# Kernel optimization log

Measured on AMD Instinct MI355X. Metric: run time of the kernel, lower is better.

The kernel has to match this reference:

```python
import jax, jax.numpy as jnp
import numpy as np

B, L, DK, DV, H = 2, 2048, 512, 512, 8
DH_K = DK // H  # 64
DH_V = DV // H  # 64


def setup_inputs() -> dict:
    key = jax.random.key(0)
    ks = jax.random.split(key, 6)
    scale_w = 1.0 / np.sqrt(DK)
    return {
        "keys": jax.random.normal(ks[0], (B, L, DK), dtype=jnp.float32),
        "queries": jax.random.normal(ks[1], (B, L, DK), dtype=jnp.float32),
        "values": jax.random.normal(ks[2], (B, L, DV), dtype=jnp.float32),
        "WQ": jax.random.normal(ks[3], (H, DK, DH_K), dtype=jnp.float32) * scale_w,
        "WK": jax.random.normal(ks[4], (H, DK, DH_K), dtype=jnp.float32) * scale_w,
        "WV": jax.random.normal(ks[5], (H, DV, DH_V), dtype=jnp.float32) * scale_w,
    }


def reference(keys, queries, values, WQ, WK, WV):
    # Per-head projections, vectorized over all H heads at once.
    Q = jnp.einsum('bld,hde->bhle', queries, WQ)   # [B,H,Lq,dh]
    K = jnp.einsum('bld,hde->bhle', keys, WK)      # [B,H,Lk,dh]
    V = jnp.einsum('bld,hde->bhle', values, WV)    # [B,H,Lk,dv_h]
    Lk = keys.shape[1]
    # NOTE: original scales by sqrt(seq_len_k), not sqrt(head_dim).
    y = jnp.einsum('bhqe,bhke->bhqk', Q, K) / jnp.sqrt(jnp.float32(Lk))
    # NOTE: original applies softmax over torch dim=1 of [B,Lq,Lk],
    # i.e. the QUERY axis (axis=2 here in [B,H,Lq,Lk]).
    z = jax.nn.softmax(y, axis=2)
    out = jnp.einsum('bhqk,bhke->bhqe', z, V)      # [B,H,Lq,dv_h]
    # Concat heads on the feature dim (same order as torch.concat(..., 2)).
    Bq, Hh, Lq, Dh = out.shape
    return out.transpose(0, 2, 1, 3).reshape(Bq, Lq, Hh * Dh)
```

## Files before the change

kernel.cpp:

```cpp
#include <hip/hip_runtime.h>
#include <hip/hip_bf16.h>

#define LL 2048
#define DM 512
#define SCALE 0.02209708691207961f

typedef unsigned short u16;
typedef __attribute__((ext_vector_type(8))) short short8;
typedef __attribute__((ext_vector_type(4))) short short4v;
typedef __attribute__((ext_vector_type(4))) float f32x4;

#define XAQ_OFF 0u
#define XAK_OFF 2097152u
#define WB_OFF  4194304u
#define QA_OFF  4980736u
#define KA_OFF  7077888u
#define VT_OFF  9175040u
#define VB_OFF  11272192u

__device__ __forceinline__ u16 f2bf(float f) {
  union { float f; unsigned u; } v; v.f = f;
  unsigned r = v.u + 0x7fff + ((v.u >> 16) & 1);
  return (u16)(r >> 16);
}
__device__ __forceinline__ float bf2f(u16 u) {
  union { unsigned u; float f; } v; v.u = ((unsigned)u) << 16; return v.f;
}
__device__ __forceinline__ size_t frag_idx(int bh, int t64, int w, int c, int lane) {
  return ((((size_t)(bh * 32 + t64) * 4 + w) * 2 + c) * 64 + lane) * 8;
}
__device__ __forceinline__ size_t vb_idx(int bh, int kt, int w, int et, int lane) {
  return ((((size_t)(bh * 32 + kt) * 4 + w) * 4 + et) * 64 + lane) * 4;
}

__global__ __launch_bounds__(256) void prep_kernel(
    const float* __restrict__ queries, const float* __restrict__ keys,
    const float* __restrict__ WQ, const float* __restrict__ WK,
    const float* __restrict__ WV, u16* __restrict__ wsb) {
  int t = threadIdx.x;
  if (blockIdx.x < 2048) {
    size_t c = (size_t)blockIdx.x * 256 + t;
    int tens = (int)(c >> 18);
    size_t off = (c & 262143u) * 8;
    int b  = (int)(off >> 20);
    int l  = (int)((off >> 9) & 2047);
    int d8 = (int)((off & 511) >> 3);
    int kt = d8 >> 2, quad = d8 & 3;
    const float* src = (tens ? keys : queries) + off;
    float4 a = *(const float4*)(src);
    float4 bb = *(const float4*)(src + 4);
    short8 o;
    o[0] = (short)f2bf(a.x); o[1] = (short)f2bf(a.y);
    o[2] = (short)f2bf(a.z); o[3] = (short)f2bf(a.w);
    o[4] = (short)f2bf(bb.x); o[5] = (short)f2bf(bb.y);
    o[6] = (short)f2bf(bb.z); o[7] = (short)f2bf(bb.w);
    size_t dst = (tens ? XAK_OFF : XAQ_OFF) +
        ((((size_t)b * 128 + (l >> 4)) * 16 + kt) * 64 + (quad * 16 + (l & 15))) * 8;
    *(short8*)(wsb + dst) = o;
  } else {
    int c2 = (blockIdx.x - 2048) * 256 + t;
    int lane = c2 & 63;
    int nt = (c2 >> 6) & 3;
    int kt = (c2 >> 8) & 15;
    int h  = (c2 >> 12) & 7;
    int z  = c2 >> 15;
    int quad = lane >> 4, l16 = lane & 15;
    const float* W = (z == 0) ? WQ : (z == 1) ? WK : WV;
    const float* src = W + ((size_t)h * DM + kt * 32 + quad * 8) * 64 + nt * 16 + l16;
    short8 o;
#pragma unroll
    for (int j = 0; j < 8; ++j) o[j] = (short)f2bf(src[(size_t)j * 64]);
    *(short8*)(wsb + WB_OFF + (size_t)c2 * 8) = o;
  }
}

__global__ __launch_bounds__(256) void proj_kernel(const float* __restrict__ values,
                                                   u16* __restrict__ wsb) {
  int t = threadIdx.x;
  int lane = t & 63, w = t >> 6, quad = lane >> 4, l16 = lane & 15;
  int z = blockIdx.z, bh = blockIdx.y, b = bh >> 3, h = bh & 7;
  int QT = blockIdx.x, qbase = QT * 64;

  const u16* Bw = wsb + WB_OFF + ((size_t)(z * 8 + h) * 16) * 4 * 64 * 8;
  __shared__ __align__(16) short As[64 * 40];

  f32x4 acc[4];
#pragma unroll
  for (int nt = 0; nt < 4; ++nt) acc[nt] = (f32x4){0.f, 0.f, 0.f, 0.f};

  if (z < 2) {
    const u16* Ab = wsb + ((z == 0) ? XAQ_OFF : XAK_OFF) +
        (((size_t)b * 128 + (qbase >> 4) + w) * 16) * 64 * 8;
#pragma unroll 4
    for (int kt = 0; kt < 16; ++kt) {
      short8 a = *(const short8*)(Ab + ((size_t)kt * 64 + lane) * 8);
#pragma unroll
      for (int nt = 0; nt < 4; ++nt) {
        short8 bb = *(const short8*)(Bw + (((size_t)kt * 4 + nt) * 64 + lane) * 8);
        acc[nt] = __builtin_amdgcn_mfma_f32_16x16x32_bf16(a, bb, acc[nt], 0, 0, 0);
      }
    }
  } else {
    const float* inbase = values + ((size_t)b * LL + qbase) * DM;
    for (int kt = 0; kt < 16; ++kt) {
      __syncthreads();
#pragma unroll
      for (int rep = 0; rep < 2; ++rep) {
        int f4 = t + rep * 256;
        int row = f4 >> 3, c4 = f4 & 7;
        float4 v = *(const float4*)(inbase + (size_t)row * DM + kt * 32 + c4 * 4);
        short* dst = &As[row * 40 + c4 * 4];
        dst[0] = (short)f2bf(v.x); dst[1] = (short)f2bf(v.y);
        dst[2] = (short)f2bf(v.z); dst[3] = (short)f2bf(v.w);
      }
      __syncthreads();
      short8 a = *(const short8*)&As[(w * 16 + l16) * 40 + quad * 8];
#pragma unroll
      for (int nt = 0; nt < 4; ++nt) {
        short8 bb = *(const short8*)(Bw + (((size_t)kt * 4 + nt) * 64 + lane) * 8);
        acc[nt] = __builtin_amdgcn_mfma_f32_16x16x32_bf16(a, bb, acc[nt], 0, 0, 0);
      }
    }
  }

  if (z < 2) {
    u16* base = wsb + ((z == 0) ? QA_OFF : KA_OFF);
    float sc = (z == 0) ? SCALE : 1.0f;
#pragma unroll
    for (int nt = 0; nt < 4; ++nt) {
      int c = nt >> 1;
      int quadp = (nt & 1) * 2 + (l16 >> 3);
      int j = l16 & 7;
#pragma unroll
      for (int r = 0; r < 4; ++r) {
        int lanep = quadp * 16 + quad * 4 + r;
        base[frag_idx(bh, QT, w, c, lanep) + j] = f2bf(acc[nt][r] * sc);
      }
    }
  } else {
    u16* og = wsb + VT_OFF + (size_t)bh * 64 * LL;
#pragma unroll
    for (int nt = 0; nt < 4; ++nt)
#pragma unroll
      for (int r = 0; r < 4; ++r)
        og[(size_t)(nt * 16 + l16) * LL + qbase + w * 16 + quad * 4 + r] = f2bf(acc[nt][r]);
  }
}

__global__ __launch_bounds__(256) void stats_kernel(u16* __restrict__ wsb) {
  int t = threadIdx.x;
  int lane = t & 63, w = t >> 6, quad = lane >> 4, l16 = lane & 15;
  int bh = blockIdx.y;
  int KT = blockIdx.x;

  short8 ka[4][2];
#pragma unroll
  for (int mt = 0; mt < 4; ++mt)
#pragma unroll
    for (int c = 0; c < 2; ++c)
      ka[mt][c] = *(const short8*)(wsb + KA_OFF + frag_idx(bh, KT, mt, c, lane));

  float rs[4][4];
#pragma unroll
  for (int mt = 0; mt < 4; ++mt)
#pragma unroll
    for (int r = 0; r < 4; ++r) rs[mt][r] = 0.f;

  for (int qt = 0; qt < 32; ++qt) {
    short8 qb0 = *(const short8*)(wsb + QA_OFF + frag_idx(bh, qt, w, 0, lane));
    short8 qb1 = *(const short8*)(wsb + QA_OFF + frag_idx(bh, qt, w, 1, lane));
#pragma unroll
    for (int mt = 0; mt < 4; ++mt) {
      f32x4 y = (f32x4){0.f, 0.f, 0.f, 0.f};
      y = __builtin_amdgcn_mfma_f32_16x16x32_bf16(ka[mt][0], qb0, y, 0, 0, 0);
      y = __builtin_amdgcn_mfma_f32_16x16x32_bf16(ka[mt][1], qb1, y, 0, 0, 0);
#pragma unroll
      for (int r = 0; r < 4; ++r) rs[mt][r] += __expf(y[r]);
    }
  }
#pragma unroll
  for (int mt = 0; mt < 4; ++mt)
#pragma unroll
    for (int r = 0; r < 4; ++r) {
      rs[mt][r] += __shfl_xor(rs[mt][r], 1);
      rs[mt][r] += __shfl_xor(rs[mt][r], 2);
      rs[mt][r] += __shfl_xor(rs[mt][r], 4);
      rs[mt][r] += __shfl_xor(rs[mt][r], 8);
    }

  __shared__ float Sred[4][64];
  __shared__ float Ss[64];
  if (l16 == 0) {
#pragma unroll
    for (int mt = 0; mt < 4; ++mt)
#pragma unroll
      for (int r = 0; r < 4; ++r)
        Sred[w][mt * 16 + quad * 4 + r] = rs[mt][r];
  }
  __syncthreads();
  if (t < 64) Ss[t] = 1.0f / (Sred[0][t] + Sred[1][t] + Sred[2][t] + Sred[3][t]);
  __syncthreads();

#pragma unroll
  for (int rep = 0; rep < 2; ++rep) {
    int f8 = t + rep * 256;
    int e = f8 >> 3, c8 = f8 & 7;
    const u16* src = wsb + VT_OFF + ((size_t)bh * 64 + e) * LL + KT * 64 + c8 * 8;
    short8 v = *(const short8*)src;
    float sv[8];
#pragma unroll
    for (int i = 0; i < 8; ++i) sv[i] = bf2f((u16)v[i]) * Ss[c8 * 8 + i];
    int wv = c8 >> 1, et = e >> 4;
#pragma unroll
    for (int g = 0; g < 2; ++g) {
      short4v o;
#pragma unroll
      for (int j = 0; j < 4; ++j) o[j] = (short)f2bf(sv[g * 4 + j]);
      int lanep = ((c8 & 1) * 2 + g) * 16 + (e & 15);
      *(short4v*)(wsb + VB_OFF + vb_idx(bh, KT, wv, et, lanep)) = o;
    }
  }
}

__global__ __launch_bounds__(256, 2) void attn_kernel(const u16* __restrict__ wsb,
                                                      float* __restrict__ out) {
  int t = threadIdx.x;
  int lane = t & 63, w = t >> 6, quad = lane >> 4, l16 = lane & 15;
  int bh = blockIdx.y, b = bh >> 3, h = bh & 7;
  int QT = blockIdx.x, qbase = QT * 64;

  short8 qf[4][2];
#pragma unroll
  for (int nt = 0; nt < 4; ++nt)
#pragma unroll
    for (int c = 0; c < 2; ++c)
      qf[nt][c] = *(const short8*)(wsb + QA_OFF + frag_idx(bh, QT, nt, c, lane));

  f32x4 oacc[4][4];
#pragma unroll
  for (int nt = 0; nt < 4; ++nt)
#pragma unroll
    for (int et = 0; et < 4; ++et) oacc[nt][et] = (f32x4){0.f, 0.f, 0.f, 0.f};

  for (int kt = 0; kt < 32; ++kt) {
    short8 ka0 = *(const short8*)(wsb + KA_OFF + frag_idx(bh, kt, w, 0, lane));
    short8 ka1 = *(const short8*)(wsb + KA_OFF + frag_idx(bh, kt, w, 1, lane));
    short4v vb[4];
#pragma unroll
    for (int et = 0; et < 4; ++et)
      vb[et] = *(const short4v*)(wsb + VB_OFF + vb_idx(bh, kt, w, et, lane));

#pragma unroll
    for (int nt = 0; nt < 4; ++nt) {
      f32x4 y = (f32x4){0.f, 0.f, 0.f, 0.f};
      y = __builtin_amdgcn_mfma_f32_16x16x32_bf16(ka0, qf[nt][0], y, 0, 0, 0);
      y = __builtin_amdgcn_mfma_f32_16x16x32_bf16(ka1, qf[nt][1], y, 0, 0, 0);
      short4v pa;
#pragma unroll
      for (int r = 0; r < 4; ++r) pa[r] = (short)f2bf(__expf(y[r]));
#pragma unroll
      for (int et = 0; et < 4; ++et)
        oacc[nt][et] = __builtin_amdgcn_mfma_f32_16x16x16bf16_1k(pa, vb[et], oacc[nt][et], 0, 0, 0);
    }
  }

  __shared__ float red[4][64][68];
#pragma unroll
  for (int nt = 0; nt < 4; ++nt)
#pragma unroll
    for (int et = 0; et < 4; ++et)
#pragma unroll
      for (int r = 0; r < 4; ++r)
        red[w][nt * 16 + quad * 4 + r][et * 16 + l16] = oacc[nt][et][r];
  __syncthreads();
  float* og = out + ((size_t)b * LL + qbase + w * 16) * 512 + h * 64;
#pragma unroll
  for (int i = 0; i < 16; ++i) {
    float s = red[0][w * 16 + i][lane] + red[1][w * 16 + i][lane] +
              red[2][w * 16 + i][lane] + red[3][w * 16 + i][lane];
    og[(size_t)i * 512 + lane] = s;
  }
}

extern "C" void kernel_launch(void* const* d_in, const int* in_sizes, int n_in,
                              void* d_out, int out_size, void* d_ws, size_t ws_size,
                              hipStream_t stream) {
  const float* keys    = (const float*)d_in[0];
  const float* queries = (const float*)d_in[1];
  const float* values  = (const float*)d_in[2];
  const float* WQ      = (const float*)d_in[3];
  const float* WK      = (const float*)d_in[4];
  const float* WV      = (const float*)d_in[5];
  float* out = (float*)d_out;
  u16* wsb = (u16*)d_ws;

  prep_kernel<<<dim3(2048 + 384), 256, 0, stream>>>(queries, keys, WQ, WK, WV, wsb);
  proj_kernel<<<dim3(32, 16, 3), 256, 0, stream>>>(values, wsb);
  stats_kernel<<<dim3(32, 16), 256, 0, stream>>>(wsb);
  attn_kernel<<<dim3(32, 16), 256, 0, stream>>>(wsb, out);
}
```

Baseline: 147.5 us.

## Pre-convert values to bf16 fragments and stage projection outputs through LDS

The prep kernel now converts all three inputs (queries, keys, values) into bf16 MFMA A-fragment layout using an LDS transpose with coalesced loads and stores. This lets the V projection use the same register-only MFMA loop instead of per-k-tile LDS staging with barriers. Projection outputs are staged in shared memory so Q/K fragments are written as short8 vectors and V goes straight into the VB fragment layout. The stats kernel then only rescales VB in place, and the VT intermediate is dropped. This trades scattered 2-byte stores and an extra transpose pass for one more LDS round trip and barrier in the projection epilogue.

```diff
diff --git a/kernel.cpp b/kernel.cpp
--- a/kernel.cpp
+++ b/kernel.cpp
@@ -12,10 +12,10 @@
 
 #define XAQ_OFF 0u
 #define XAK_OFF 2097152u
-#define WB_OFF  4194304u
-#define QA_OFF  4980736u
-#define KA_OFF  7077888u
-#define VT_OFF  9175040u
+#define XAV_OFF 4194304u
+#define WB_OFF  6291456u
+#define QA_OFF  7077888u
+#define KA_OFF  9175040u
 #define VB_OFF  11272192u
 
 __device__ __forceinline__ u16 f2bf(float f) {
@@ -35,30 +35,40 @@
 
 __global__ __launch_bounds__(256) void prep_kernel(
     const float* __restrict__ queries, const float* __restrict__ keys,
-    const float* __restrict__ WQ, const float* __restrict__ WK,
-    const float* __restrict__ WV, u16* __restrict__ wsb) {
-  int t = threadIdx.x;
-  if (blockIdx.x < 2048) {
-    size_t c = (size_t)blockIdx.x * 256 + t;
-    int tens = (int)(c >> 18);
-    size_t off = (c & 262143u) * 8;
-    int b  = (int)(off >> 20);
-    int l  = (int)((off >> 9) & 2047);
-    int d8 = (int)((off & 511) >> 3);
-    int kt = d8 >> 2, quad = d8 & 3;
-    const float* src = (tens ? keys : queries) + off;
-    float4 a = *(const float4*)(src);
-    float4 bb = *(const float4*)(src + 4);
-    short8 o;
-    o[0] = (short)f2bf(a.x); o[1] = (short)f2bf(a.y);
-    o[2] = (short)f2bf(a.z); o[3] = (short)f2bf(a.w);
-    o[4] = (short)f2bf(bb.x); o[5] = (short)f2bf(bb.y);
-    o[6] = (short)f2bf(bb.z); o[7] = (short)f2bf(bb.w);
-    size_t dst = (tens ? XAK_OFF : XAQ_OFF) +
-        ((((size_t)b * 128 + (l >> 4)) * 16 + kt) * 64 + (quad * 16 + (l & 15))) * 8;
-    *(short8*)(wsb + dst) = o;
+    const float* __restrict__ values, const float* __restrict__ WQ,
+    const float* __restrict__ WK, const float* __restrict__ WV,
+    u16* __restrict__ wsb) {
+  int t = threadIdx.x;
+  int blk = blockIdx.x;
+  if (blk < 768) {
+    int tens = blk >> 8;
+    int grp  = blk & 255;
+    const float* src = (tens == 0 ? queries : tens == 1 ? keys : values) +
+                       (size_t)grp * 16 * 512;
+    __shared__ __align__(16) u16 Xs[16][520];
+#pragma unroll
+    for (int rep = 0; rep < 8; ++rep) {
+      int f4 = t + rep * 256;
+      int row = f4 >> 7, c4 = f4 & 127;
+      float4 v = *(const float4*)(src + (size_t)row * 512 + c4 * 4);
+      short4v o;
+      o[0] = (short)f2bf(v.x); o[1] = (short)f2bf(v.y);
+      o[2] = (short)f2bf(v.z); o[3] = (short)f2bf(v.w);
+      *(short4v*)&Xs[row][c4 * 4] = o;
+    }
+    __syncthreads();
+    u16* dst = wsb + (tens == 0 ? XAQ_OFF : tens == 1 ? XAK_OFF : XAV_OFF) +
+               (size_t)grp * 16 * 64 * 8;
+#pragma unroll
+    for (int rep = 0; rep < 4; ++rep) {
+      int o = t + rep * 256;
+      int kt = o >> 6, lane = o & 63;
+      int quad = lane >> 4, l16 = lane & 15;
+      short8 v = *(const short8*)&Xs[l16][kt * 32 + quad * 8];
+      *(short8*)(dst + (size_t)o * 8) = v;
+    }
   } else {
-    int c2 = (blockIdx.x - 2048) * 256 + t;
+    int c2 = (blk - 768) * 256 + t;
     int lane = c2 & 63;
     int nt = (c2 >> 6) & 3;
     int kt = (c2 >> 8) & 15;
@@ -74,76 +84,58 @@
   }
 }
 
-__global__ __launch_bounds__(256) void proj_kernel(const float* __restrict__ values,
-                                                   u16* __restrict__ wsb) {
+__global__ __launch_bounds__(256) void proj_kernel(u16* __restrict__ wsb) {
   int t = threadIdx.x;
   int lane = t & 63, w = t >> 6, quad = lane >> 4, l16 = lane & 15;
   int z = blockIdx.z, bh = blockIdx.y, b = bh >> 3, h = bh & 7;
-  int QT = blockIdx.x, qbase = QT * 64;
+  int QT = blockIdx.x;
 
   const u16* Bw = wsb + WB_OFF + ((size_t)(z * 8 + h) * 16) * 4 * 64 * 8;
-  __shared__ __align__(16) short As[64 * 40];
+  const u16* Ab = wsb + (z == 0 ? XAQ_OFF : z == 1 ? XAK_OFF : XAV_OFF) +
+      (((size_t)b * 128 + QT * 4 + w) * 16) * 64 * 8;
 
   f32x4 acc[4];
 #pragma unroll
   for (int nt = 0; nt < 4; ++nt) acc[nt] = (f32x4){0.f, 0.f, 0.f, 0.f};
 
+#pragma unroll 4
+  for (int kt = 0; kt < 16; ++kt) {
+    short8 a = *(const short8*)(Ab + ((size_t)kt * 64 + lane) * 8);
+#pragma unroll
+    for (int nt = 0; nt < 4; ++nt) {
+      short8 bb = *(const short8*)(Bw + (((size_t)kt * 4 + nt) * 64 + lane) * 8);
+      acc[nt] = __builtin_amdgcn_mfma_f32_16x16x32_bf16(a, bb, acc[nt], 0, 0, 0);
+    }
+  }
+
+  __shared__ float Cs[64][68];
+  float sc = (z == 0) ? SCALE : 1.0f;
+#pragma unroll
+  for (int nt = 0; nt < 4; ++nt)
+#pragma unroll
+    for (int r = 0; r < 4; ++r)
+      Cs[w * 16 + quad * 4 + r][nt * 16 + l16] = acc[nt][r] * sc;
+  __syncthreads();
+
   if (z < 2) {
-    const u16* Ab = wsb + ((z == 0) ? XAQ_OFF : XAK_OFF) +
-        (((size_t)b * 128 + (qbase >> 4) + w) * 16) * 64 * 8;
-#pragma unroll 4
-    for (int kt = 0; kt < 16; ++kt) {
-      short8 a = *(const short8*)(Ab + ((size_t)kt * 64 + lane) * 8);
-#pragma unroll
-      for (int nt = 0; nt < 4; ++nt) {
-        short8 bb = *(const short8*)(Bw + (((size_t)kt * 4 + nt) * 64 + lane) * 8);
-        acc[nt] = __builtin_amdgcn_mfma_f32_16x16x32_bf16(a, bb, acc[nt], 0, 0, 0);
-      }
+    u16* base = wsb + (z == 0 ? QA_OFF : KA_OFF);
+#pragma unroll
+    for (int c = 0; c < 2; ++c) {
+      const float* srcr = &Cs[w * 16 + l16][c * 32 + quad * 8];
+      short8 o;
+#pragma unroll
+      for (int j = 0; j < 8; ++j) o[j] = (short)f2bf(srcr[j]);
+      *(short8*)(base + frag_idx(bh, QT, w, c, lane)) = o;
     }
   } else {
-    const float* inbase = values + ((size_t)b * LL + qbase) * DM;
-    for (int kt = 0; kt < 16; ++kt) {
-      __syncthreads();
-#pragma unroll
-      for (int rep = 0; rep < 2; ++rep) {
-        int f4 = t + rep * 256;
-        int row = f4 >> 3, c4 = f4 & 7;
-        float4 v = *(const float4*)(inbase + (size_t)row * DM + kt * 32 + c4 * 4);
-        short* dst = &As[row * 40 + c4 * 4];
-        dst[0] = (short)f2bf(v.x); dst[1] = (short)f2bf(v.y);
-        dst[2] = (short)f2bf(v.z); dst[3] = (short)f2bf(v.w);
-      }
-      __syncthreads();
-      short8 a = *(const short8*)&As[(w * 16 + l16) * 40 + quad * 8];
-#pragma unroll
-      for (int nt = 0; nt < 4; ++nt) {
-        short8 bb = *(const short8*)(Bw + (((size_t)kt * 4 + nt) * 64 + lane) * 8);
-        acc[nt] = __builtin_amdgcn_mfma_f32_16x16x32_bf16(a, bb, acc[nt], 0, 0, 0);
-      }
-    }
-  }
-
-  if (z < 2) {
-    u16* base = wsb + ((z == 0) ? QA_OFF : KA_OFF);
-    float sc = (z == 0) ? SCALE : 1.0f;
-#pragma unroll
-    for (int nt = 0; nt < 4; ++nt) {
-      int c = nt >> 1;
-      int quadp = (nt & 1) * 2 + (l16 >> 3);
-      int j = l16 & 7;
-#pragma unroll
-      for (int r = 0; r < 4; ++r) {
-        int lanep = quadp * 16 + quad * 4 + r;
-        base[frag_idx(bh, QT, w, c, lanep) + j] = f2bf(acc[nt][r] * sc);
-      }
-    }
-  } else {
-    u16* og = wsb + VT_OFF + (size_t)bh * 64 * LL;
-#pragma unroll
-    for (int nt = 0; nt < 4; ++nt)
-#pragma unroll
-      for (int r = 0; r < 4; ++r)
-        og[(size_t)(nt * 16 + l16) * LL + qbase + w * 16 + quad * 4 + r] = f2bf(acc[nt][r]);
+#pragma unroll
+    for (int et = 0; et < 4; ++et) {
+      short4v o;
+#pragma unroll
+      for (int j = 0; j < 4; ++j)
+        o[j] = (short)f2bf(Cs[w * 16 + quad * 4 + j][et * 16 + l16]);
+      *(short4v*)(wsb + VB_OFF + vb_idx(bh, QT, w, et, lane)) = o;
+    }
   }
 }
 
@@ -202,23 +194,13 @@
   __syncthreads();
 
 #pragma unroll
-  for (int rep = 0; rep < 2; ++rep) {
-    int f8 = t + rep * 256;
-    int e = f8 >> 3, c8 = f8 & 7;
-    const u16* src = wsb + VT_OFF + ((size_t)bh * 64 + e) * LL + KT * 64 + c8 * 8;
-    short8 v = *(const short8*)src;
-    float sv[8];
-#pragma unroll
-    for (int i = 0; i < 8; ++i) sv[i] = bf2f((u16)v[i]) * Ss[c8 * 8 + i];
-    int wv = c8 >> 1, et = e >> 4;
-#pragma unroll
-    for (int g = 0; g < 2; ++g) {
-      short4v o;
-#pragma unroll
-      for (int j = 0; j < 4; ++j) o[j] = (short)f2bf(sv[g * 4 + j]);
-      int lanep = ((c8 & 1) * 2 + g) * 16 + (e & 15);
-      *(short4v*)(wsb + VB_OFF + vb_idx(bh, KT, wv, et, lanep)) = o;
-    }
+  for (int et = 0; et < 4; ++et) {
+    u16* p = wsb + VB_OFF + vb_idx(bh, KT, w, et, lane);
+    short4v v = *(short4v*)p;
+#pragma unroll
+    for (int j = 0; j < 4; ++j)
+      v[j] = (short)f2bf(bf2f((u16)v[j]) * Ss[w * 16 + quad * 4 + j]);
+    *(short4v*)p = v;
   }
 }
 
@@ -294,8 +276,8 @@
   float* out = (float*)d_out;
   u16* wsb = (u16*)d_ws;
 
-  prep_kernel<<<dim3(2048 + 384), 256, 0, stream>>>(queries, keys, WQ, WK, WV, wsb);
-  proj_kernel<<<dim3(32, 16, 3), 256, 0, stream>>>(values, wsb);
+  prep_kernel<<<dim3(768 + 384), 256, 0, stream>>>(queries, keys, values, WQ, WK, WV, wsb);
+  proj_kernel<<<dim3(32, 16, 3), 256, 0, stream>>>(wsb);
   stats_kernel<<<dim3(32, 16), 256, 0, stream>>>(wsb);
   attn_kernel<<<dim3(32, 16), 256, 0, stream>>>(wsb, out);
 }
```

Measured after the change: 143.4 us. -2.8%, faster.
